# Kernel optimization log

Measured on AMD Instinct MI355X. Metric: run time of the kernel, lower is better.

## Reference

```python
import jax, jax.numpy as jnp
import numpy as np
from math import sqrt

B, P, D = 4, 2048, 1024
H, DK = 16, 64  # n_heads, d_keys


def setup_inputs() -> dict:
    key = jax.random.key(0)
    ks = jax.random.split(key, 6)
    s = 1.0 / sqrt(D)
    return {
        "target_embedding": jax.random.normal(ks[0], (B, P, D), dtype=jnp.float32),
        "Wq": jax.random.normal(ks[1], (D, H * DK), dtype=jnp.float32) * s,
        "bq": jnp.zeros((H * DK,), dtype=jnp.float32),
        "Wk": jax.random.normal(ks[2], (D, H * DK), dtype=jnp.float32) * s,
        "bk": jnp.zeros((H * DK,), dtype=jnp.float32),
        "Wv": jax.random.normal(ks[3], (D, H * DK), dtype=jnp.float32) * s,
        "bv": jnp.zeros((H * DK,), dtype=jnp.float32),
        "Wo": jax.random.normal(ks[4], (H * DK, D), dtype=jnp.float32) * s,
        "bo": jnp.zeros((D,), dtype=jnp.float32),
    }


def reference(target_embedding, Wq, bq, Wk, bk, Wv, bv, Wo, bo):
    x = target_embedding
    b, p, _ = x.shape
    # QKV projections -> [B, P, H, DK]
    q = (x @ Wq + bq).reshape(b, p, H, DK)
    k = (x @ Wk + bk).reshape(b, p, H, DK)
    v = (x @ Wv + bv).reshape(b, p, H, DK)
    scale = 1.0 / sqrt(DK)
    scores = jnp.einsum("bphd,bqhd->bhpq", q, k)  # [B, H, P, P]
    A = jax.nn.softmax(scale * scores, axis=-1)  # dropout is identity in eval
    rep = jnp.einsum("bhpq,bqhd->bphd", A, v).reshape(b, p, H * DK)
    return rep @ Wo + bo
```

## Files before the change

kernel.cpp:

```cpp
#include <hip/hip_runtime.h>

typedef __attribute__((ext_vector_type(8))) short short8;
typedef __attribute__((ext_vector_type(4))) float f32x4;
typedef __attribute__((ext_vector_type(4))) unsigned short ushort4v;

#define GLOBAL_AS __attribute__((address_space(1)))
#define LDS_AS    __attribute__((address_space(3)))

__device__ __forceinline__ unsigned short f2bf(float f) {
    unsigned int u = __float_as_uint(f);
    u += 0x7fffu + ((u >> 16) & 1u);
    return (unsigned short)(u >> 16);
}

__device__ __forceinline__ float fexp2(float x) {
    return __builtin_amdgcn_exp2f(x);
}

__device__ __forceinline__ void async_cp16(void* lds, const void* g) {
    __builtin_amdgcn_global_load_lds((GLOBAL_AS unsigned int*)g,
                                     (LDS_AS unsigned int*)lds, 16, 0, 0);
}

#define SCL2E 0.18033688011112042591999058512524f

__global__ void convert_x_kernel(const float* __restrict__ X,
                                 unsigned short* __restrict__ Xb) {
    int i = (blockIdx.x * 256 + threadIdx.x) * 4;
    float4 v = *(const float4*)&X[i];
    ushort4v o;
    o.x = f2bf(v.x); o.y = f2bf(v.y); o.z = f2bf(v.z); o.w = f2bf(v.w);
    *(ushort4v*)&Xb[i] = o;
}

__global__ void transpose_w_kernel(const float* __restrict__ Wq,
                                   const float* __restrict__ Wk,
                                   const float* __restrict__ Wv,
                                   const float* __restrict__ Wo,
                                   unsigned short* __restrict__ Wts) {
    __shared__ float tile[32][33];
    const int z = blockIdx.z;
    const float* src = (z == 0) ? Wq : (z == 1) ? Wk : (z == 2) ? Wv : Wo;
    unsigned short* dst = Wts + z * 1048576;
    const int tx = threadIdx.x, ty = threadIdx.y;
    const int x0 = blockIdx.x * 32, y0 = blockIdx.y * 32;
#pragma unroll
    for (int i = 0; i < 32; i += 8)
        tile[ty + i][tx] = src[(y0 + ty + i) * 1024 + x0 + tx];
    __syncthreads();
#pragma unroll
    for (int i = 0; i < 32; i += 8)
        dst[(x0 + ty + i) * 1024 + y0 + tx] = f2bf(tile[tx][ty + i]);
}

__global__ void transpose_v_kernel(const unsigned short* __restrict__ V,
                                   unsigned short* __restrict__ Vt) {
    __shared__ unsigned short tile[32][33];
    const int bh = blockIdx.z;
    const int p0 = blockIdx.x * 32, d0 = blockIdx.y * 32;
    const unsigned short* src = V + bh * (2048 * 64);
    unsigned short* dst = Vt + bh * (2048 * 64);
    const int tx = threadIdx.x, ty = threadIdx.y;
#pragma unroll
    for (int i = 0; i < 32; i += 8)
        tile[ty + i][tx] = src[(p0 + ty + i) * 64 + d0 + tx];
    __syncthreads();
#pragma unroll
    for (int i = 0; i < 32; i += 8)
        dst[(d0 + ty + i) * 2048 + p0 + tx] = tile[tx][ty + i];
}

__device__ __forceinline__ void gemm_mainloop_128(
    const unsigned short* __restrict__ A, const unsigned short* __restrict__ Bt,
    int m0, int n0, unsigned short* As, unsigned short* Bs, f32x4 acc[4][4]) {
    const int tid = threadIdx.x;
    const int lane = tid & 63;
    const int wave = tid >> 6;
    const int wr = wave >> 1, wc = wave & 1;
    const int c = lane & 15, quad = lane >> 4;

#pragma unroll
    for (int mt = 0; mt < 4; ++mt)
#pragma unroll
        for (int nt = 0; nt < 4; ++nt)
            acc[mt][nt] = (f32x4)0.0f;

    for (int k0 = 0; k0 < 1024; k0 += 32) {
#pragma unroll
        for (int i = 0; i < 2; ++i) {
            int s = tid + 256 * i;
            int r = s >> 2, gp = s & 3;
            int g = gp ^ ((r >> 1) & 3);
            async_cp16(&As[s * 8], &A[(m0 + r) * 1024 + k0 + g * 8]);
        }
#pragma unroll
        for (int i = 0; i < 2; ++i) {
            int s = tid + 256 * i;
            int r = s >> 2, gp = s & 3;
            int g = gp ^ ((r >> 1) & 3);
            async_cp16(&Bs[s * 8], &Bt[(n0 + r) * 1024 + k0 + g * 8]);
        }
        asm volatile("s_waitcnt vmcnt(0)" ::: "memory");
        __syncthreads();

        short8 af[4], bf[4];
#pragma unroll
        for (int mt = 0; mt < 4; ++mt) {
            int r = wr * 64 + mt * 16 + c;
            int gp = quad ^ ((r >> 1) & 3);
            af[mt] = *(const short8*)&As[r * 32 + gp * 8];
        }
#pragma unroll
        for (int nt = 0; nt < 4; ++nt) {
            int r = wc * 64 + nt * 16 + c;
            int gp = quad ^ ((r >> 1) & 3);
            bf[nt] = *(const short8*)&Bs[r * 32 + gp * 8];
        }
#pragma unroll
        for (int mt = 0; mt < 4; ++mt)
#pragma unroll
            for (int nt = 0; nt < 4; ++nt)
                acc[mt][nt] = __builtin_amdgcn_mfma_f32_16x16x32_bf16(
                    af[mt], bf[nt], acc[mt][nt], 0, 0, 0);
        __syncthreads();
    }
}

__global__ __launch_bounds__(256, 3) void gemm_qkv_kernel(
    const unsigned short* __restrict__ Xb, const unsigned short* __restrict__ Wts,
    const float* __restrict__ bq, const float* __restrict__ bk,
    const float* __restrict__ bv, unsigned short* __restrict__ Qb,
    unsigned short* __restrict__ Kb, unsigned short* __restrict__ Vb) {
    __shared__ __align__(16) unsigned short As[128 * 32];
    __shared__ __align__(16) unsigned short Bs[128 * 32];
    const int z = blockIdx.z;
    const unsigned short* Bt = Wts + z * 1048576;
    const float* bias = (z == 0) ? bq : (z == 1) ? bk : bv;
    const int m0 = blockIdx.y * 128, n0 = blockIdx.x * 128;
    f32x4 acc[4][4];
    gemm_mainloop_128(Xb, Bt, m0, n0, As, Bs, acc);

    const int lane = threadIdx.x & 63, wave = threadIdx.x >> 6;
    const int wr = wave >> 1, wc = wave & 1;
    const int c = lane & 15, quad = lane >> 4;
    unsigned short* dst = (z == 0) ? Qb : (z == 1) ? Kb : Vb;
    const float qscale = (z == 0) ? SCL2E : 1.0f;
#pragma unroll
    for (int nt = 0; nt < 4; ++nt) {
        int col = n0 + wc * 64 + nt * 16 + c;
        float bb = bias[col];
        int h = col >> 6, dk = col & 63;
#pragma unroll
        for (int mt = 0; mt < 4; ++mt) {
#pragma unroll
            for (int r = 0; r < 4; ++r) {
                int row = m0 + wr * 64 + mt * 16 + quad * 4 + r;
                int b = row >> 11, p = row & 2047;
                float v = (acc[mt][nt][r] + bb) * qscale;
                dst[((b * 16 + h) * 2048 + p) * 64 + dk] = f2bf(v);
            }
        }
    }
}

__device__ __forceinline__ void load_kv_regs(
    const unsigned short* __restrict__ Kbh, const unsigned short* __restrict__ Vbh,
    int k0, int tid, short8 kr[2], short8 vr[2]) {
#pragma unroll
    for (int i = 0; i < 2; ++i) {
        int s = tid + 256 * i;
        int r = s >> 3, gp = s & 7;
        int g = gp ^ (r & 7);
        kr[i] = *(const short8*)&Kbh[(k0 + r) * 64 + g * 8];
        vr[i] = *(const short8*)&Vbh[r * 2048 + k0 + g * 8];
    }
}

__global__ __launch_bounds__(256, 3) void attn_kernel(
    const unsigned short* __restrict__ Q, const unsigned short* __restrict__ K,
    const unsigned short* __restrict__ Vt, unsigned short* __restrict__ rep) {
    __shared__ __align__(16) unsigned short Ks[2][64 * 64];
    __shared__ __align__(16) unsigned short Vs[2][64 * 64];
    __shared__ __align__(16) unsigned short Ps[4][32 * 72];
    const int tid = threadIdx.x, lane = tid & 63, wave = tid >> 6;
    const int c = lane & 15, quad = lane >> 4;
    const int bh = blockIdx.y;
    const int q0 = blockIdx.x * 128 + wave * 32;
    const unsigned short* Qbh = Q + bh * (2048 * 64);
    const unsigned short* Kbh = K + bh * (2048 * 64);
    const unsigned short* Vbh = Vt + bh * (64 * 2048);

    short8 qf[2][2];
#pragma unroll
    for (int t = 0; t < 2; ++t)
#pragma unroll
        for (int ks = 0; ks < 2; ++ks)
            qf[t][ks] = *(const short8*)&Qbh[(q0 + t * 16 + c) * 64 + ks * 32 + quad * 8];

    short8 kr[2], vr[2];
    load_kv_regs(Kbh, Vbh, 0, tid, kr, vr);

    f32x4 o[2][4];
    float lpart[2][4];
#pragma unroll
    for (int t = 0; t < 2; ++t) {
#pragma unroll
        for (int d = 0; d < 4; ++d) o[t][d] = (f32x4)0.0f;
#pragma unroll
        for (int r = 0; r < 4; ++r) lpart[t][r] = 0.0f;
    }

#pragma unroll 2
    for (int it = 0; it < 32; ++it) {
        const int buf = it & 1;
        unsigned short* Ksb = &Ks[buf][0];
        unsigned short* Vsb = &Vs[buf][0];
#pragma unroll
        for (int i = 0; i < 2; ++i) {
            int s = tid + 256 * i;
            *(short8*)&Ksb[s * 8] = kr[i];
            *(short8*)&Vsb[s * 8] = vr[i];
        }
        __syncthreads();
        if (it < 31)
            load_kv_regs(Kbh, Vbh, (it + 1) * 64, tid, kr, vr);

        short8 kf[4][2];
#pragma unroll
        for (int nt = 0; nt < 4; ++nt)
#pragma unroll
            for (int ks = 0; ks < 2; ++ks) {
                int r = nt * 16 + c;
                int gp2 = (quad + 4 * ks) ^ (r & 7);
                kf[nt][ks] = *(const short8*)&Ksb[r * 64 + gp2 * 8];
            }

        f32x4 sc[2][4];
#pragma unroll
        for (int t = 0; t < 2; ++t)
#pragma unroll
            for (int nt = 0; nt < 4; ++nt) {
                f32x4 z4 = (f32x4)0.0f;
                z4 = __builtin_amdgcn_mfma_f32_16x16x32_bf16(qf[t][0], kf[nt][0], z4, 0, 0, 0);
                sc[t][nt] = __builtin_amdgcn_mfma_f32_16x16x32_bf16(qf[t][1], kf[nt][1], z4, 0, 0, 0);
            }

#pragma unroll
        for (int t = 0; t < 2; ++t)
#pragma unroll
            for (int nt = 0; nt < 4; ++nt)
#pragma unroll
                for (int r = 0; r < 4; ++r) {
                    float p = fexp2(sc[t][nt][r]);
                    lpart[t][r] += p;
                    Ps[wave][(t * 16 + quad * 4 + r) * 72 + nt * 16 + c] = f2bf(p);
                }
        asm volatile("s_waitcnt lgkmcnt(0)" ::: "memory");

        short8 pf[2][2];
#pragma unroll
        for (int t = 0; t < 2; ++t)
#pragma unroll
            for (int ks = 0; ks < 2; ++ks)
                pf[t][ks] = *(const short8*)&Ps[wave][(t * 16 + c) * 72 + ks * 32 + quad * 8];
#pragma unroll
        for (int dkt = 0; dkt < 4; ++dkt) {
#pragma unroll
            for (int ks = 0; ks < 2; ++ks) {
                int r = dkt * 16 + c;
                int gp2 = (quad + 4 * ks) ^ (r & 7);
                short8 vf = *(const short8*)&Vsb[r * 64 + gp2 * 8];
#pragma unroll
                for (int t = 0; t < 2; ++t)
                    o[t][dkt] = __builtin_amdgcn_mfma_f32_16x16x32_bf16(
                        pf[t][ks], vf, o[t][dkt], 0, 0, 0);
            }
        }
    }

    const int b = bh >> 4, h = bh & 15;
#pragma unroll
    for (int t = 0; t < 2; ++t) {
        float inv[4];
#pragma unroll
        for (int r = 0; r < 4; ++r) {
            float l = lpart[t][r];
            l += __shfl_xor(l, 1);
            l += __shfl_xor(l, 2);
            l += __shfl_xor(l, 4);
            l += __shfl_xor(l, 8);
            inv[r] = 1.0f / l;
        }
#pragma unroll
        for (int dkt = 0; dkt < 4; ++dkt)
#pragma unroll
            for (int r = 0; r < 4; ++r)
                rep[(b * 2048 + q0 + t * 16 + quad * 4 + r) * 1024 + h * 64 + dkt * 16 + c] =
                    f2bf(o[t][dkt][r] * inv[r]);
    }
}

__global__ __launch_bounds__(256, 3) void gemm_out_kernel(
    const unsigned short* __restrict__ rep, const unsigned short* __restrict__ Wot,
    const float* __restrict__ bo, float* __restrict__ out) {
    __shared__ __align__(16) unsigned short As[128 * 32];
    __shared__ __align__(16) unsigned short Bs[128 * 32];
    const int m0 = blockIdx.y * 128, n0 = blockIdx.x * 128;
    f32x4 acc[4][4];
    gemm_mainloop_128(rep, Wot, m0, n0, As, Bs, acc);
    const int lane = threadIdx.x & 63, wave = threadIdx.x >> 6;
    const int wr = wave >> 1, wc = wave & 1;
    const int c = lane & 15, quad = lane >> 4;
#pragma unroll
    for (int nt = 0; nt < 4; ++nt) {
        int col = n0 + wc * 64 + nt * 16 + c;
        float bb = bo[col];
#pragma unroll
        for (int mt = 0; mt < 4; ++mt) {
            int row = m0 + wr * 64 + mt * 16 + quad * 4;
#pragma unroll
            for (int r = 0; r < 4; ++r)
                out[(row + r) * 1024 + col] = acc[mt][nt][r] + bb;
        }
    }
}

extern "C" void kernel_launch(void* const* d_in, const int* in_sizes, int n_in,
                              void* d_out, int out_size, void* d_ws, size_t ws_size,
                              hipStream_t stream) {
    (void)in_sizes; (void)n_in; (void)out_size; (void)ws_size;
    const float* X  = (const float*)d_in[0];
    const float* Wq = (const float*)d_in[1];
    const float* bq = (const float*)d_in[2];
    const float* Wk = (const float*)d_in[3];
    const float* bk = (const float*)d_in[4];
    const float* Wv = (const float*)d_in[5];
    const float* bv = (const float*)d_in[6];
    const float* Wo = (const float*)d_in[7];
    const float* bo = (const float*)d_in[8];
    float* out = (float*)d_out;

    char* ws = (char*)d_ws;
    unsigned short* Xb   = (unsigned short*)(ws);
    unsigned short* Wts  = (unsigned short*)(ws + (16u << 20));
    unsigned short* Qb   = (unsigned short*)(ws + (24u << 20));
    unsigned short* Kb   = (unsigned short*)(ws + (40u << 20));
    unsigned short* Vb   = (unsigned short*)(ws + (56u << 20));
    unsigned short* Vtb  = (unsigned short*)(ws);
    unsigned short* repb = (unsigned short*)(ws + (56u << 20));

    convert_x_kernel<<<8192, 256, 0, stream>>>(X, Xb);
    transpose_w_kernel<<<dim3(32, 32, 4), dim3(32, 8), 0, stream>>>(Wq, Wk, Wv, Wo, Wts);
    gemm_qkv_kernel<<<dim3(8, 64, 3), 256, 0, stream>>>(Xb, Wts, bq, bk, bv, Qb, Kb, Vb);
    transpose_v_kernel<<<dim3(64, 2, 64), dim3(32, 8), 0, stream>>>(Vb, Vtb);
    attn_kernel<<<dim3(16, 64), 256, 0, stream>>>(Qb, Kb, Vtb, repb);
    gemm_out_kernel<<<dim3(8, 64), 256, 0, stream>>>(repb, Wts + 3 * 1048576, bo, out);
}
```

Before: 308.7 us.

## Compute transposed scores so P stays in registers for PV MFMA

Swaps operands in the QK^T MFMA so each lane holds score columns matching the B-operand layout of the 16x16x16 bf16 MFMA. Probabilities are then packed to bf16 in registers and fed straight into the PV product, removing the per-wave LDS round-trip for P and its waitcnt. The output is staged through LDS so rep is written with 16-byte row stores, and row-sum reduction shrinks to two shuffles. Trade-offs: twice as many smaller MFMAs for PV, launch bounds lowered from 3 to 2 blocks per SM, and the unroll-2 pragma is dropped.

```diff
diff --git a/kernel.cpp b/kernel.cpp
--- a/kernel.cpp
+++ b/kernel.cpp
@@ -1,6 +1,7 @@
 #include <hip/hip_runtime.h>
 
 typedef __attribute__((ext_vector_type(8))) short short8;
+typedef __attribute__((ext_vector_type(4))) short short4v;
 typedef __attribute__((ext_vector_type(4))) float f32x4;
 typedef __attribute__((ext_vector_type(4))) unsigned short ushort4v;
 
@@ -176,12 +177,15 @@
     }
 }
 
-__global__ __launch_bounds__(256, 3) void attn_kernel(
+__device__ __forceinline__ unsigned int pack_bf16(float a, float b) {
+    return (unsigned int)f2bf(a) | ((unsigned int)f2bf(b) << 16);
+}
+
+__global__ __launch_bounds__(256, 2) void attn_kernel(
     const unsigned short* __restrict__ Q, const unsigned short* __restrict__ K,
     const unsigned short* __restrict__ Vt, unsigned short* __restrict__ rep) {
     __shared__ __align__(16) unsigned short Ks[2][64 * 64];
     __shared__ __align__(16) unsigned short Vs[2][64 * 64];
-    __shared__ __align__(16) unsigned short Ps[4][32 * 72];
     const int tid = threadIdx.x, lane = tid & 63, wave = tid >> 6;
     const int c = lane & 15, quad = lane >> 4;
     const int bh = blockIdx.y;
@@ -201,16 +205,12 @@
     load_kv_regs(Kbh, Vbh, 0, tid, kr, vr);
 
     f32x4 o[2][4];
-    float lpart[2][4];
-#pragma unroll
-    for (int t = 0; t < 2; ++t) {
+    float lpart[2] = {0.0f, 0.0f};
+#pragma unroll
+    for (int t = 0; t < 2; ++t)
 #pragma unroll
         for (int d = 0; d < 4; ++d) o[t][d] = (f32x4)0.0f;
-#pragma unroll
-        for (int r = 0; r < 4; ++r) lpart[t][r] = 0.0f;
-    }
-
-#pragma unroll 2
+
     for (int it = 0; it < 32; ++it) {
         const int buf = it & 1;
         unsigned short* Ksb = &Ks[buf][0];
@@ -235,68 +235,73 @@
                 kf[nt][ks] = *(const short8*)&Ksb[r * 64 + gp2 * 8];
             }
 
-        f32x4 sc[2][4];
-#pragma unroll
-        for (int t = 0; t < 2; ++t)
+        short4v pfrag[4][2];
+#pragma unroll
+        for (int t = 0; t < 2; ++t) {
 #pragma unroll
             for (int nt = 0; nt < 4; ++nt) {
                 f32x4 z4 = (f32x4)0.0f;
-                z4 = __builtin_amdgcn_mfma_f32_16x16x32_bf16(qf[t][0], kf[nt][0], z4, 0, 0, 0);
-                sc[t][nt] = __builtin_amdgcn_mfma_f32_16x16x32_bf16(qf[t][1], kf[nt][1], z4, 0, 0, 0);
+                z4 = __builtin_amdgcn_mfma_f32_16x16x32_bf16(kf[nt][0], qf[t][0], z4, 0, 0, 0);
+                z4 = __builtin_amdgcn_mfma_f32_16x16x32_bf16(kf[nt][1], qf[t][1], z4, 0, 0, 0);
+                float p0 = fexp2(z4[0]), p1 = fexp2(z4[1]);
+                float p2 = fexp2(z4[2]), p3 = fexp2(z4[3]);
+                lpart[t] += (p0 + p1) + (p2 + p3);
+                unsigned int u01 = pack_bf16(p0, p1);
+                unsigned int u23 = pack_bf16(p2, p3);
+                short4v pf;
+                pf[0] = (short)(u01 & 0xffff); pf[1] = (short)(u01 >> 16);
+                pf[2] = (short)(u23 & 0xffff); pf[3] = (short)(u23 >> 16);
+                pfrag[nt][t] = pf;
             }
-
-#pragma unroll
-        for (int t = 0; t < 2; ++t)
-#pragma unroll
-            for (int nt = 0; nt < 4; ++nt)
-#pragma unroll
-                for (int r = 0; r < 4; ++r) {
-                    float p = fexp2(sc[t][nt][r]);
-                    lpart[t][r] += p;
-                    Ps[wave][(t * 16 + quad * 4 + r) * 72 + nt * 16 + c] = f2bf(p);
-                }
-        asm volatile("s_waitcnt lgkmcnt(0)" ::: "memory");
-
-        short8 pf[2][2];
-#pragma unroll
-        for (int t = 0; t < 2; ++t)
-#pragma unroll
-            for (int ks = 0; ks < 2; ++ks)
-                pf[t][ks] = *(const short8*)&Ps[wave][(t * 16 + c) * 72 + ks * 32 + quad * 8];
+        }
+
 #pragma unroll
         for (int dkt = 0; dkt < 4; ++dkt) {
-#pragma unroll
-            for (int ks = 0; ks < 2; ++ks) {
-                int r = dkt * 16 + c;
-                int gp2 = (quad + 4 * ks) ^ (r & 7);
-                short8 vf = *(const short8*)&Vsb[r * 64 + gp2 * 8];
+            int r = dkt * 16 + c;
+#pragma unroll
+            for (int kt = 0; kt < 4; ++kt) {
+                int gbase = 2 * kt + (quad >> 1);
+                int g = gbase ^ (r & 7);
+                int eloff = g * 8 + (quad & 1) * 4;
+                short4v vf4 = *(const short4v*)&Vsb[r * 64 + eloff];
 #pragma unroll
                 for (int t = 0; t < 2; ++t)
-                    o[t][dkt] = __builtin_amdgcn_mfma_f32_16x16x32_bf16(
-                        pf[t][ks], vf, o[t][dkt], 0, 0, 0);
+                    o[t][dkt] = __builtin_amdgcn_mfma_f32_16x16x16bf16_1k(
+                        vf4, pfrag[kt][t], o[t][dkt], 0, 0, 0);
             }
         }
     }
 
+    float inv[2];
+#pragma unroll
+    for (int t = 0; t < 2; ++t) {
+        float l = lpart[t];
+        l += __shfl_xor(l, 16);
+        l += __shfl_xor(l, 32);
+        inv[t] = 1.0f / l;
+    }
+
+    __syncthreads();
+    unsigned short* ob = ((unsigned short*)Ks) + wave * 2304;
+#pragma unroll
+    for (int t = 0; t < 2; ++t) {
+#pragma unroll
+        for (int dkt = 0; dkt < 4; ++dkt) {
+            unsigned int u01 = pack_bf16(o[t][dkt][0] * inv[t], o[t][dkt][1] * inv[t]);
+            unsigned int u23 = pack_bf16(o[t][dkt][2] * inv[t], o[t][dkt][3] * inv[t]);
+            short4v frag;
+            frag[0] = (short)(u01 & 0xffff); frag[1] = (short)(u01 >> 16);
+            frag[2] = (short)(u23 & 0xffff); frag[3] = (short)(u23 >> 16);
+            *(short4v*)&ob[(t * 16 + c) * 72 + dkt * 16 + quad * 4] = frag;
+        }
+    }
     const int b = bh >> 4, h = bh & 15;
 #pragma unroll
-    for (int t = 0; t < 2; ++t) {
-        float inv[4];
-#pragma unroll
-        for (int r = 0; r < 4; ++r) {
-            float l = lpart[t][r];
-            l += __shfl_xor(l, 1);
-            l += __shfl_xor(l, 2);
-            l += __shfl_xor(l, 4);
-            l += __shfl_xor(l, 8);
-            inv[r] = 1.0f / l;
-        }
-#pragma unroll
-        for (int dkt = 0; dkt < 4; ++dkt)
-#pragma unroll
-            for (int r = 0; r < 4; ++r)
-                rep[(b * 2048 + q0 + t * 16 + quad * 4 + r) * 1024 + h * 64 + dkt * 16 + c] =
-                    f2bf(o[t][dkt][r] * inv[r]);
+    for (int pass = 0; pass < 4; ++pass) {
+        int q = pass * 8 + (lane >> 3);
+        int d8 = (lane & 7) * 8;
+        short8 row = *(const short8*)&ob[q * 72 + d8];
+        *(short8*)&rep[(b * 2048 + q0 + q) * 1024 + h * 64 + d8] = row;
     }
 }
 
```

Result: no change. 313.7 us (+1.6%).
